# Kernel tuning notes

Measured on AMD Instinct MI355X. Metric: run time of the kernel, lower is better.

## Reference

```python
import jax, jax.numpy as jnp
from jax import lax
import numpy as np

B, T, I, H, OUT = 4096, 168, 4, 64, 12


def setup_inputs() -> dict:
    key = jax.random.key(0)
    ks = jax.random.split(key, 14)
    s = 0.05
    return {
        "x": jax.random.normal(ks[0], (B, T, I), dtype=jnp.float32),
        # LSTM layer 0 (PyTorch gate order: i, f, g, o)
        "Wih0": jax.random.normal(ks[1], (4 * H, I), dtype=jnp.float32) * s,
        "Whh0": jax.random.normal(ks[2], (4 * H, H), dtype=jnp.float32) * s,
        "bih0": jax.random.normal(ks[3], (4 * H,), dtype=jnp.float32) * s,
        "bhh0": jax.random.normal(ks[4], (4 * H,), dtype=jnp.float32) * s,
        # LSTM layer 1
        "Wih1": jax.random.normal(ks[5], (4 * H, H), dtype=jnp.float32) * s,
        "Whh1": jax.random.normal(ks[6], (4 * H, H), dtype=jnp.float32) * s,
        "bih1": jax.random.normal(ks[7], (4 * H,), dtype=jnp.float32) * s,
        "bhh1": jax.random.normal(ks[8], (4 * H,), dtype=jnp.float32) * s,
        # FC head: Linear(64,64) -> ReLU -> Linear(64,12)
        "W1": jax.random.normal(ks[9], (64, H), dtype=jnp.float32) * s,
        "b1": jax.random.normal(ks[10], (64,), dtype=jnp.float32) * s,
        "W2": jax.random.normal(ks[11], (OUT, 64), dtype=jnp.float32) * s,
        "b2": jax.random.normal(ks[12], (OUT,), dtype=jnp.float32) * s,
    }


def _lstm_layer(x, Wih, Whh, bih, bhh):
    # x: [B, T, in]; returns hidden sequence [B, T, H]
    Bsz = x.shape[0]
    Hd = Whh.shape[1]
    # Precompute input contribution for all timesteps: [B, T, 4H]
    xg = jnp.einsum('bti,gi->btg', x, Wih) + bih + bhh

    def step(carry, xg_t):
        h, c = carry
        g = xg_t + h @ Whh.T  # [B, 4H]
        i, f, gg, o = jnp.split(g, 4, axis=-1)
        i = jax.nn.sigmoid(i)
        f = jax.nn.sigmoid(f)
        gg = jnp.tanh(gg)
        o = jax.nn.sigmoid(o)
        c = f * c + i * gg
        h = o * jnp.tanh(c)
        return (h, c), h

    h0 = jnp.zeros((Bsz, Hd), x.dtype)
    (_, _), hs = lax.scan(step, (h0, h0), jnp.swapaxes(xg, 0, 1))  # hs: [T, B, H]
    return jnp.swapaxes(hs, 0, 1)


def reference(x, Wih0, Whh0, bih0, bhh0, Wih1, Whh1, bih1, bhh1, W1, b1, W2, b2):
    # Eval-mode forward: dropout layers are identity.
    h1 = _lstm_layer(x, Wih0, Whh0, bih0, bhh0)   # [B, T, H]
    h2 = _lstm_layer(h1, Wih1, Whh1, bih1, bhh1)  # [B, T, H]
    last = h2[:, -1, :]                            # [B, H]
    z = jax.nn.relu(last @ W1.T + b1)              # [B, 64]
    out = z @ W2.T + b2                            # [B, 12]
    return out.reshape(-1, 3, 4)
```

## Files before the change

### kernel.cpp

```cpp
#include <hip/hip_runtime.h>


typedef _Float16 h8 __attribute__((ext_vector_type(8)));
typedef _Float16 h4 __attribute__((ext_vector_type(4)));
typedef float f4 __attribute__((ext_vector_type(4)));

#define ROWB 208
#define HBUF (16 * ROWB)
#define XTAB_OFF 0
#define XTAB_BYTES (169 * 256)
#define H0_OFF XTAB_BYTES
#define H1_OFF (H0_OFF + 2 * HBUF)
#define SMEM_TOTAL (H1_OFF + 2 * HBUF)

#define K1F 1.4426950408889634f
#define K2F 2.8853900817779268f

__device__ __forceinline__ float exp2_(float x) {
#if __has_builtin(__builtin_amdgcn_exp2f)
  return __builtin_amdgcn_exp2f(x);
#else
  float r; asm("v_exp_f32 %0, %1" : "=v"(r) : "v"(x)); return r;
#endif
}
__device__ __forceinline__ float rcp_(float x) {
#if __has_builtin(__builtin_amdgcn_rcpf)
  return __builtin_amdgcn_rcpf(x);
#else
  float r; asm("v_rcp_f32 %0, %1" : "=v"(r) : "v"(x)); return r;
#endif
}

__device__ __forceinline__ f4 mfma16(h8 a, h8 b, f4 c) {
  return __builtin_amdgcn_mfma_f32_16x16x32_f16(a, b, c, 0, 0, 0);
}

__device__ __forceinline__ h8 load_w8s(const float* __restrict__ p, float sc) {
  h8 r;
#pragma unroll
  for (int j = 0; j < 8; j++) r[j] = (_Float16)(p[j] * sc);
  return r;
}

__device__ __forceinline__ void lstm_act(f4 a, float& c, float& h) {
  float Ei = exp2_(-a[0]);
  float Ef = exp2_(-a[1]);
  float Eg = exp2_(a[2]);
  float Eo = exp2_(-a[3]);
  float A = 1.f + Ei, B = 1.f + Ef, C = 1.f + Eg, D = 1.f + Eo;
  float AB = A * B, CD = C * D, BD = B * D;
  float R  = rcp_(AB * CD);
  float fv = (A * CD) * R;
  float ig = (BD * (Eg - 1.f)) * R;
  float ov = (AB * C) * R;
  c = fv * c + ig;
  float r2 = rcp_(exp2_(c * K2F) + 1.f);
  h = ov * (1.f - 2.f * r2);
}

extern "C" __global__ void __launch_bounds__(512, 2)
weather_lstm_mfma6(const float* __restrict__ x,
                   const float* __restrict__ Wih0, const float* __restrict__ Whh0,
                   const float* __restrict__ bih0, const float* __restrict__ bhh0,
                   const float* __restrict__ Wih1, const float* __restrict__ Whh1,
                   const float* __restrict__ bih1, const float* __restrict__ bhh1,
                   const float* __restrict__ W1, const float* __restrict__ b1,
                   const float* __restrict__ W2, const float* __restrict__ b2,
                   float* __restrict__ out)
{
  __shared__ __align__(16) unsigned char smem[SMEM_TOTAL];
  const int tid  = threadIdx.x;
  const int lane = tid & 63;
  const int w    = tid >> 6;
  const int col  = lane & 15;
  const int quad = lane >> 4;
  const int sB   = blockIdx.x * 16;

  const int g_  = col & 3;
  const int ul_ = col >> 2;
  const float asc = (g_ == 2) ? K2F : K1F;

  h8 a0[2][3], a1i[2][2], a1h[2][2];
#pragma unroll
  for (int t = 0; t < 2; t++) {
    const int r = g_ * 64 + w * 8 + t * 4 + ul_;
#pragma unroll
    for (int f = 0; f < 2; f++) {
      a0[t][f]  = load_w8s(Whh0 + r * 64 + f * 32 + quad * 8, asc);
      a1i[t][f] = load_w8s(Wih1 + r * 64 + f * 32 + quad * 8, asc);
      a1h[t][f] = load_w8s(Whh1 + r * 64 + f * 32 + quad * 8, asc);
    }
    h8 xw = {};
    if (quad == 0) {
#pragma unroll
      for (int j = 0; j < 4; j++) xw[j] = (_Float16)(Wih0[r * 4 + j] * asc);
    }
    a0[t][2] = xw;
  }

  f4 bias0v[2], bias1v[2];
#pragma unroll
  for (int t = 0; t < 2; t++) {
#pragma unroll
    for (int reg = 0; reg < 4; reg++) {
      const int rr = reg * 64 + w * 8 + t * 4 + quad;
      const float bs = (reg == 2) ? K2F : K1F;
      bias0v[t][reg] = (bih0[rr] + bhh0[rr]) * bs;
      bias1v[t][reg] = (bih1[rr] + bhh1[rr]) * bs;
    }
  }

  for (int idx = tid; idx < SMEM_TOTAL / 4; idx += 512) ((int*)smem)[idx] = 0;
  __syncthreads();
  for (int idx = tid; idx < 16 * 168; idx += 512) {
    const int c_ = idx / 168, t_ = idx - c_ * 168;
    f4 xv = *(const f4*)(x + ((size_t)(sB + c_) * 168 + t_) * 4);
    h4 xh;
#pragma unroll
    for (int j = 0; j < 4; j++) xh[j] = (_Float16)xv[j];
    *(h4*)(smem + XTAB_OFF + t_ * 256 + c_ * 16) = xh;
  }
  __syncthreads();

  float c0[2] = {0.f, 0.f}, c1[2] = {0.f, 0.f}, hl[2] = {0.f, 0.f};
  const int bo  = col * ROWB + quad * 16;
  const int wo0 = col * ROWB + (w * 8 + quad) * 2;
  const unsigned char* xp = smem + XTAB_OFF + col * 16;

  for (int k = 0; k <= 168; k++) {
    const int kb = k & 1, kbn = kb ^ 1;
    const unsigned char* h0r = smem + H0_OFF + kbn * HBUF;
    unsigned char*       h0w = smem + H0_OFF + kb  * HBUF;
    const unsigned char* h1r = smem + H1_OFF + kb  * HBUF;
    unsigned char*       h1w = smem + H1_OFF + kbn * HBUF;

    h8 b0  = *(const h8*)(h0r + bo);
    h8 b1v = *(const h8*)(h0r + bo + 64);
    h8 bx  = *(const h8*)(xp + k * 256);
    h8 q0  = *(const h8*)(h1r + bo);
    h8 q1  = *(const h8*)(h1r + bo + 64);

    f4 A[2], C[2];
#pragma unroll
    for (int t = 0; t < 2; t++) {
      A[t] = mfma16(a0[t][0], b0, bias0v[t]);
      C[t] = mfma16(a1i[t][0], b0, bias1v[t]);
      A[t] = mfma16(a0[t][1], b1v, A[t]);
      C[t] = mfma16(a1i[t][1], b1v, C[t]);
      A[t] = mfma16(a0[t][2], bx, A[t]);
      C[t] = mfma16(a1h[t][0], q0, C[t]);
      C[t] = mfma16(a1h[t][1], q1, C[t]);
    }

    if (k < 168) {
#pragma unroll
      for (int t = 0; t < 2; t++) {
        float h0o;
        lstm_act(A[t], c0[t], h0o);
        *(_Float16*)(h0w + wo0 + t * 8) = (_Float16)h0o;
      }
    }
    if (k > 0) {
#pragma unroll
      for (int t = 0; t < 2; t++) {
        lstm_act(C[t], c1[t], hl[t]);
        *(_Float16*)(h1w + wo0 + t * 8) = (_Float16)hl[t];
      }
    }
    __syncthreads();
  }

  float* fh = (float*)smem;
#pragma unroll
  for (int t = 0; t < 2; t++)
    fh[col * 64 + (w * 8 + t * 4 + quad)] = hl[t];
  __syncthreads();

  {
    const int u = tid & 63, grp = tid >> 6;
    const float* w1r = W1 + u * 64;
    float* zl = (float*)(smem + 4096);
#pragma unroll
    for (int rep = 0; rep < 2; rep++) {
      const int s = grp + rep * 8;
      float za = b1[u];
      const float* f0 = fh + s * 64;
      for (int j = 0; j < 64; j++) za += w1r[j] * f0[j];
      zl[s * 64 + u] = fmaxf(za, 0.f);
    }
  }
  __syncthreads();

  if (tid < 192) {
    const float* zl = (const float*)(smem + 4096);
    const int s = tid / 12, o = tid - s * 12;
    float a = b2[o];
    for (int j = 0; j < 64; j++) a += W2[o * 64 + j] * zl[s * 64 + j];
    out[(sB + s) * 12 + o] = a;
  }
}

extern "C" void kernel_launch(void* const* d_in, const int* in_sizes, int n_in,
                              void* d_out, int out_size, void* d_ws, size_t ws_size,
                              hipStream_t stream) {
  (void)in_sizes; (void)n_in; (void)d_ws; (void)ws_size; (void)out_size;
  const float* x    = (const float*)d_in[0];
  const float* Wih0 = (const float*)d_in[1];
  const float* Whh0 = (const float*)d_in[2];
  const float* bih0 = (const float*)d_in[3];
  const float* bhh0 = (const float*)d_in[4];
  const float* Wih1 = (const float*)d_in[5];
  const float* Whh1 = (const float*)d_in[6];
  const float* bih1 = (const float*)d_in[7];
  const float* bhh1 = (const float*)d_in[8];
  const float* W1   = (const float*)d_in[9];
  const float* b1   = (const float*)d_in[10];
  const float* W2   = (const float*)d_in[11];
  const float* b2   = (const float*)d_in[12];

  weather_lstm_mfma6<<<dim3(256), dim3(512), 0, stream>>>(
      x, Wih0, Whh0, bih0, bhh0, Wih1, Whh1, bih1, bhh1, W1, b1, W2, b2,
      (float*)d_out);
}
```

Measured before the change: 230.7 us.

## Halve batch per block and split activation work across MFMA column halves

Each block now handles 8 sequences instead of 16, and the grid doubles to 512 blocks. MFMA columns 8-15 duplicate the batch columns, so each lane applies the LSTM activation to only one of the two tile outputs, selected by column half. This halves the serial transcendental work per lane on the recurrent critical path and spreads blocks over more CUs, with launch bounds raised to 4 blocks per CU. The cost is that half of each MFMA's output columns do redundant work, and higher occupancy may pressure registers.

```diff
diff --git a/kernel.cpp b/kernel.cpp
--- a/kernel.cpp
+++ b/kernel.cpp
@@ -6,9 +6,9 @@
 typedef float f4 __attribute__((ext_vector_type(4)));
 
 #define ROWB 208
-#define HBUF (16 * ROWB)
+#define HBUF (8 * ROWB)
 #define XTAB_OFF 0
-#define XTAB_BYTES (169 * 256)
+#define XTAB_BYTES (169 * 128)
 #define H0_OFF XTAB_BYTES
 #define H1_OFF (H0_OFF + 2 * HBUF)
 #define SMEM_TOTAL (H1_OFF + 2 * HBUF)
@@ -39,6 +39,13 @@
   h8 r;
 #pragma unroll
   for (int j = 0; j < 8; j++) r[j] = (_Float16)(p[j] * sc);
+  return r;
+}
+
+__device__ __forceinline__ f4 sel4(int hi, f4 a, f4 b) {
+  f4 r;
+#pragma unroll
+  for (int j = 0; j < 4; j++) r[j] = hi ? b[j] : a[j];
   return r;
 }
 
@@ -58,8 +65,8 @@
   h = ov * (1.f - 2.f * r2);
 }
 
-extern "C" __global__ void __launch_bounds__(512, 2)
-weather_lstm_mfma6(const float* __restrict__ x,
+extern "C" __global__ void __launch_bounds__(512, 4)
+weather_lstm_mfma7(const float* __restrict__ x,
                    const float* __restrict__ Wih0, const float* __restrict__ Whh0,
                    const float* __restrict__ bih0, const float* __restrict__ bhh0,
                    const float* __restrict__ Wih1, const float* __restrict__ Whh1,
@@ -73,8 +80,10 @@
   const int lane = tid & 63;
   const int w    = tid >> 6;
   const int col  = lane & 15;
+  const int s    = col & 7;
+  const int sel  = col >> 3;
   const int quad = lane >> 4;
-  const int sB   = blockIdx.x * 16;
+  const int sB   = blockIdx.x * 8;
 
   const int g_  = col & 3;
   const int ul_ = col >> 2;
@@ -112,20 +121,20 @@
 
   for (int idx = tid; idx < SMEM_TOTAL / 4; idx += 512) ((int*)smem)[idx] = 0;
   __syncthreads();
-  for (int idx = tid; idx < 16 * 168; idx += 512) {
+  for (int idx = tid; idx < 8 * 168; idx += 512) {
     const int c_ = idx / 168, t_ = idx - c_ * 168;
     f4 xv = *(const f4*)(x + ((size_t)(sB + c_) * 168 + t_) * 4);
     h4 xh;
 #pragma unroll
     for (int j = 0; j < 4; j++) xh[j] = (_Float16)xv[j];
-    *(h4*)(smem + XTAB_OFF + t_ * 256 + c_ * 16) = xh;
-  }
-  __syncthreads();
-
-  float c0[2] = {0.f, 0.f}, c1[2] = {0.f, 0.f}, hl[2] = {0.f, 0.f};
-  const int bo  = col * ROWB + quad * 16;
-  const int wo0 = col * ROWB + (w * 8 + quad) * 2;
-  const unsigned char* xp = smem + XTAB_OFF + col * 16;
+    *(h4*)(smem + XTAB_OFF + t_ * 128 + c_ * 16) = xh;
+  }
+  __syncthreads();
+
+  float c0 = 0.f, c1 = 0.f, hl = 0.f;
+  const int bo = s * ROWB + quad * 16;
+  const int wo = s * ROWB + (w * 8 + sel * 4 + quad) * 2;
+  const unsigned char* xp = smem + XTAB_OFF + s * 16;
 
   for (int k = 0; k <= 168; k++) {
     const int kb = k & 1, kbn = kb ^ 1;
@@ -136,7 +145,7 @@
 
     h8 b0  = *(const h8*)(h0r + bo);
     h8 b1v = *(const h8*)(h0r + bo + 64);
-    h8 bx  = *(const h8*)(xp + k * 256);
+    h8 bx  = *(const h8*)(xp + k * 128);
     h8 q0  = *(const h8*)(h1r + bo);
     h8 q1  = *(const h8*)(h1r + bo + 64);
 
@@ -153,50 +162,40 @@
     }
 
     if (k < 168) {
-#pragma unroll
-      for (int t = 0; t < 2; t++) {
-        float h0o;
-        lstm_act(A[t], c0[t], h0o);
-        *(_Float16*)(h0w + wo0 + t * 8) = (_Float16)h0o;
-      }
+      f4 G = sel4(sel, A[0], A[1]);
+      float h0o;
+      lstm_act(G, c0, h0o);
+      *(_Float16*)(h0w + wo) = (_Float16)h0o;
     }
     if (k > 0) {
-#pragma unroll
-      for (int t = 0; t < 2; t++) {
-        lstm_act(C[t], c1[t], hl[t]);
-        *(_Float16*)(h1w + wo0 + t * 8) = (_Float16)hl[t];
-      }
+      f4 G = sel4(sel, C[0], C[1]);
+      lstm_act(G, c1, hl);
+      *(_Float16*)(h1w + wo) = (_Float16)hl;
     }
     __syncthreads();
   }
 
   float* fh = (float*)smem;
-#pragma unroll
-  for (int t = 0; t < 2; t++)
-    fh[col * 64 + (w * 8 + t * 4 + quad)] = hl[t];
+  fh[s * 64 + (w * 8 + sel * 4 + quad)] = hl;
   __syncthreads();
 
   {
     const int u = tid & 63, grp = tid >> 6;
+    float za = b1[u];
     const float* w1r = W1 + u * 64;
+    const float* f0 = fh + grp * 64;
+    for (int j = 0; j < 64; j++) za += w1r[j] * f0[j];
     float* zl = (float*)(smem + 4096);
-#pragma unroll
-    for (int rep = 0; rep < 2; rep++) {
-      const int s = grp + rep * 8;
-      float za = b1[u];
-      const float* f0 = fh + s * 64;
-      for (int j = 0; j < 64; j++) za += w1r[j] * f0[j];
-      zl[s * 64 + u] = fmaxf(za, 0.f);
-    }
-  }
-  __syncthreads();
-
-  if (tid < 192) {
+    zl[grp * 64 + u] = fmaxf(za, 0.f);
+  }
+  __syncthreads();
+
+  if (tid < 96) {
     const float* zl = (const float*)(smem + 4096);
-    const int s = tid / 12, o = tid - s * 12;
+    const int s2 = tid / 12, o = tid - s2 * 12;
     float a = b2[o];
-    for (int j = 0; j < 64; j++) a += W2[o * 64 + j] * zl[s * 64 + j];
-    out[(sB + s) * 12 + o] = a;
+    for (int j = 0; j < 64; j++) a += W2[o * 64 + j] * zl[s2 * 64 + j];
+    out[(sB + s2) * 12 + o] = a;
   }
 }
 
@@ -218,7 +217,7 @@
   const float* W2   = (const float*)d_in[11];
   const float* b2   = (const float*)d_in[12];
 
-  weather_lstm_mfma6<<<dim3(256), dim3(512), 0, stream>>>(
+  weather_lstm_mfma7<<<dim3(512), dim3(512), 0, stream>>>(
       x, Wih0, Whh0, bih0, bhh0, Wih1, Whh1, bih1, bhh1, W1, b1, W2, b2,
       (float*)d_out);
 }
```

Measured after the change: 260.6 us. 1.13x slower.

## Split LSTM layers across warp groups with LDS flag handoff instead of barriers

Applied to the files above, without the earlier changes.

The two LSTM layers now run on separate warp groups: four waves compute layer 0 and four compute layer 1. Each wave handles all four gates for 16 hidden units. The per-step block-wide __syncthreads is replaced by per-wave progress flags in shared memory that consumers spin on, with a four-deep ring buffer for layer-0 hidden states so layer 0 can run ahead of layer 1. The aim is to pipeline the layers and cut barrier stalls. In exchange it adds spin-wait polling overhead, depends on LDS memory ordering through volatile accesses and block fences, and gives each wave a longer serial dependency chain per step.

```diff
diff --git a/kernel.cpp b/kernel.cpp
--- a/kernel.cpp
+++ b/kernel.cpp
@@ -10,8 +10,9 @@
 #define XTAB_OFF 0
 #define XTAB_BYTES (169 * 256)
 #define H0_OFF XTAB_BYTES
-#define H1_OFF (H0_OFF + 2 * HBUF)
-#define SMEM_TOTAL (H1_OFF + 2 * HBUF)
+#define H1_OFF (H0_OFF + 4 * HBUF)
+#define FLAG_OFF (H1_OFF + 2 * HBUF)
+#define SMEM_TOTAL (FLAG_OFF + 32)
 
 #define K1F 1.4426950408889634f
 #define K2F 2.8853900817779268f
@@ -40,6 +41,15 @@
 #pragma unroll
   for (int j = 0; j < 8; j++) r[j] = (_Float16)(p[j] * sc);
   return r;
+}
+
+__device__ __forceinline__ void spin_min_ge(volatile const int* f, int target) {
+  for (;;) {
+    int a = f[0], b = f[1], c = f[2], d = f[3];
+    int m = min(min(a, b), min(c, d));
+    if (m >= target) break;
+    __builtin_amdgcn_s_sleep(1);
+  }
 }
 
 __device__ __forceinline__ void lstm_act(f4 a, float& c, float& h) {
@@ -59,7 +69,7 @@
 }
 
 extern "C" __global__ void __launch_bounds__(512, 2)
-weather_lstm_mfma6(const float* __restrict__ x,
+weather_lstm_mfma8(const float* __restrict__ x,
                    const float* __restrict__ Wih0, const float* __restrict__ Whh0,
                    const float* __restrict__ bih0, const float* __restrict__ bhh0,
                    const float* __restrict__ Wih1, const float* __restrict__ Whh1,
@@ -76,39 +86,8 @@
   const int quad = lane >> 4;
   const int sB   = blockIdx.x * 16;
 
-  const int g_  = col & 3;
-  const int ul_ = col >> 2;
-  const float asc = (g_ == 2) ? K2F : K1F;
-
-  h8 a0[2][3], a1i[2][2], a1h[2][2];
-#pragma unroll
-  for (int t = 0; t < 2; t++) {
-    const int r = g_ * 64 + w * 8 + t * 4 + ul_;
-#pragma unroll
-    for (int f = 0; f < 2; f++) {
-      a0[t][f]  = load_w8s(Whh0 + r * 64 + f * 32 + quad * 8, asc);
-      a1i[t][f] = load_w8s(Wih1 + r * 64 + f * 32 + quad * 8, asc);
-      a1h[t][f] = load_w8s(Whh1 + r * 64 + f * 32 + quad * 8, asc);
-    }
-    h8 xw = {};
-    if (quad == 0) {
-#pragma unroll
-      for (int j = 0; j < 4; j++) xw[j] = (_Float16)(Wih0[r * 4 + j] * asc);
-    }
-    a0[t][2] = xw;
-  }
-
-  f4 bias0v[2], bias1v[2];
-#pragma unroll
-  for (int t = 0; t < 2; t++) {
-#pragma unroll
-    for (int reg = 0; reg < 4; reg++) {
-      const int rr = reg * 64 + w * 8 + t * 4 + quad;
-      const float bs = (reg == 2) ? K2F : K1F;
-      bias0v[t][reg] = (bih0[rr] + bhh0[rr]) * bs;
-      bias1v[t][reg] = (bih1[rr] + bhh1[rr]) * bs;
-    }
-  }
+  volatile int* p0w = (volatile int*)(smem + FLAG_OFF);
+  volatile int* p1w = (volatile int*)(smem + FLAG_OFF + 16);
 
   for (int idx = tid; idx < SMEM_TOTAL / 4; idx += 512) ((int*)smem)[idx] = 0;
   __syncthreads();
@@ -122,58 +101,145 @@
   }
   __syncthreads();
 
-  float c0[2] = {0.f, 0.f}, c1[2] = {0.f, 0.f}, hl[2] = {0.f, 0.f};
-  const int bo  = col * ROWB + quad * 16;
-  const int wo0 = col * ROWB + (w * 8 + quad) * 2;
-  const unsigned char* xp = smem + XTAB_OFF + col * 16;
-
-  for (int k = 0; k <= 168; k++) {
-    const int kb = k & 1, kbn = kb ^ 1;
-    const unsigned char* h0r = smem + H0_OFF + kbn * HBUF;
-    unsigned char*       h0w = smem + H0_OFF + kb  * HBUF;
-    const unsigned char* h1r = smem + H1_OFF + kb  * HBUF;
-    unsigned char*       h1w = smem + H1_OFF + kbn * HBUF;
-
-    h8 b0  = *(const h8*)(h0r + bo);
-    h8 b1v = *(const h8*)(h0r + bo + 64);
-    h8 bx  = *(const h8*)(xp + k * 256);
-    h8 q0  = *(const h8*)(h1r + bo);
-    h8 q1  = *(const h8*)(h1r + bo + 64);
-
-    f4 A[2], C[2];
-#pragma unroll
-    for (int t = 0; t < 2; t++) {
-      A[t] = mfma16(a0[t][0], b0, bias0v[t]);
-      C[t] = mfma16(a1i[t][0], b0, bias1v[t]);
-      A[t] = mfma16(a0[t][1], b1v, A[t]);
-      C[t] = mfma16(a1i[t][1], b1v, C[t]);
-      A[t] = mfma16(a0[t][2], bx, A[t]);
-      C[t] = mfma16(a1h[t][0], q0, C[t]);
-      C[t] = mfma16(a1h[t][1], q1, C[t]);
-    }
-
-    if (k < 168) {
-#pragma unroll
-      for (int t = 0; t < 2; t++) {
-        float h0o;
-        lstm_act(A[t], c0[t], h0o);
-        *(_Float16*)(h0w + wo0 + t * 8) = (_Float16)h0o;
-      }
-    }
-    if (k > 0) {
-#pragma unroll
-      for (int t = 0; t < 2; t++) {
-        lstm_act(C[t], c1[t], hl[t]);
-        *(_Float16*)(h1w + wo0 + t * 8) = (_Float16)hl[t];
-      }
-    }
-    __syncthreads();
-  }
+  const int wl = w & 3;
+  const int u0 = wl * 16;
+  const int uu = u0 + quad * 4;
+  const int bo = col * ROWB + quad * 16;
+  const int wo = col * ROWB + uu * 2;
+
+  float hout[4] = {0.f, 0.f, 0.f, 0.f};
+
+  if (w < 4) {
+    h8 aW[4][2], aX[4];
+    f4 bias[4];
+#pragma unroll
+    for (int g = 0; g < 4; ++g) {
+      const float sc = (g == 2) ? K2F : K1F;
+      const int r = g * 64 + u0 + col;
+#pragma unroll
+      for (int f = 0; f < 2; ++f)
+        aW[g][f] = load_w8s(Whh0 + r * 64 + f * 32 + quad * 8, sc);
+      h8 xw = {};
+      if (quad == 0) {
+#pragma unroll
+        for (int j = 0; j < 4; ++j) xw[j] = (_Float16)(Wih0[r * 4 + j] * sc);
+      }
+      aX[g] = xw;
+#pragma unroll
+      for (int j = 0; j < 4; ++j)
+        bias[g][j] = (bih0[g * 64 + uu + j] + bhh0[g * 64 + uu + j]) * sc;
+    }
+
+    float cc[4] = {0.f, 0.f, 0.f, 0.f};
+    const unsigned char* xp = smem + XTAB_OFF + col * 16;
+
+    for (int k = 0; k < 168; ++k) {
+      spin_min_ge(p0w, k);
+      if (k >= 4) spin_min_ge(p1w, k - 3);
+
+      const unsigned char* h0r = smem + H0_OFF + ((k - 1) & 3) * HBUF;
+      unsigned char*       h0wp = smem + H0_OFF + (k & 3) * HBUF;
+
+      h8 b0  = *(const h8*)(h0r + bo);
+      h8 b1v = *(const h8*)(h0r + bo + 64);
+      h8 bx  = *(const h8*)(xp + k * 256);
+
+      f4 A0 = mfma16(aW[0][0], b0, bias[0]);
+      f4 A1 = mfma16(aW[1][0], b0, bias[1]);
+      f4 A2 = mfma16(aW[2][0], b0, bias[2]);
+      f4 A3 = mfma16(aW[3][0], b0, bias[3]);
+      A0 = mfma16(aW[0][1], b1v, A0);
+      A1 = mfma16(aW[1][1], b1v, A1);
+      A2 = mfma16(aW[2][1], b1v, A2);
+      A3 = mfma16(aW[3][1], b1v, A3);
+      A0 = mfma16(aX[0], bx, A0);
+      A1 = mfma16(aX[1], bx, A1);
+      A2 = mfma16(aX[2], bx, A2);
+      A3 = mfma16(aX[3], bx, A3);
+
+      h4 hv;
+#pragma unroll
+      for (int j = 0; j < 4; ++j) {
+        f4 G; G[0] = A0[j]; G[1] = A1[j]; G[2] = A2[j]; G[3] = A3[j];
+        float ho;
+        lstm_act(G, cc[j], ho);
+        hv[j] = (_Float16)ho;
+      }
+      *(h4*)(h0wp + wo) = hv;
+
+      __threadfence_block();
+      if (lane == 0) p0w[wl] = k + 1;
+    }
+  } else {
+    h8 aI[4][2], aH[4][2];
+    f4 bias[4];
+#pragma unroll
+    for (int g = 0; g < 4; ++g) {
+      const float sc = (g == 2) ? K2F : K1F;
+      const int r = g * 64 + u0 + col;
+#pragma unroll
+      for (int f = 0; f < 2; ++f) {
+        aI[g][f] = load_w8s(Wih1 + r * 64 + f * 32 + quad * 8, sc);
+        aH[g][f] = load_w8s(Whh1 + r * 64 + f * 32 + quad * 8, sc);
+      }
+#pragma unroll
+      for (int j = 0; j < 4; ++j)
+        bias[g][j] = (bih1[g * 64 + uu + j] + bhh1[g * 64 + uu + j]) * sc;
+    }
+
+    float cc[4] = {0.f, 0.f, 0.f, 0.f};
+
+    for (int k = 0; k < 168; ++k) {
+      spin_min_ge(p1w, k);
+      spin_min_ge(p0w, k + 1);
+
+      const unsigned char* h0r  = smem + H0_OFF + (k & 3) * HBUF;
+      const unsigned char* h1r  = smem + H1_OFF + ((k - 1) & 1) * HBUF;
+      unsigned char*       h1wp = smem + H1_OFF + (k & 1) * HBUF;
+
+      h8 b0  = *(const h8*)(h0r + bo);
+      h8 b1v = *(const h8*)(h0r + bo + 64);
+      h8 q0  = *(const h8*)(h1r + bo);
+      h8 q1  = *(const h8*)(h1r + bo + 64);
+
+      f4 C0 = mfma16(aI[0][0], b0, bias[0]);
+      f4 C1 = mfma16(aI[1][0], b0, bias[1]);
+      f4 C2 = mfma16(aI[2][0], b0, bias[2]);
+      f4 C3 = mfma16(aI[3][0], b0, bias[3]);
+      C0 = mfma16(aI[0][1], b1v, C0);
+      C1 = mfma16(aI[1][1], b1v, C1);
+      C2 = mfma16(aI[2][1], b1v, C2);
+      C3 = mfma16(aI[3][1], b1v, C3);
+      C0 = mfma16(aH[0][0], q0, C0);
+      C1 = mfma16(aH[1][0], q0, C1);
+      C2 = mfma16(aH[2][0], q0, C2);
+      C3 = mfma16(aH[3][0], q0, C3);
+      C0 = mfma16(aH[0][1], q1, C0);
+      C1 = mfma16(aH[1][1], q1, C1);
+      C2 = mfma16(aH[2][1], q1, C2);
+      C3 = mfma16(aH[3][1], q1, C3);
+
+      h4 hv;
+#pragma unroll
+      for (int j = 0; j < 4; ++j) {
+        f4 G; G[0] = C0[j]; G[1] = C1[j]; G[2] = C2[j]; G[3] = C3[j];
+        lstm_act(G, cc[j], hout[j]);
+        hv[j] = (_Float16)hout[j];
+      }
+      *(h4*)(h1wp + wo) = hv;
+
+      __threadfence_block();
+      if (lane == 0) p1w[wl] = k + 1;
+    }
+  }
+
+  __syncthreads();
 
   float* fh = (float*)smem;
-#pragma unroll
-  for (int t = 0; t < 2; t++)
-    fh[col * 64 + (w * 8 + t * 4 + quad)] = hl[t];
+  if (w >= 4) {
+    f4 hv; hv[0] = hout[0]; hv[1] = hout[1]; hv[2] = hout[2]; hv[3] = hout[3];
+    *(f4*)(fh + col * 64 + uu) = hv;
+  }
   __syncthreads();
 
   {
@@ -181,22 +247,22 @@
     const float* w1r = W1 + u * 64;
     float* zl = (float*)(smem + 4096);
 #pragma unroll
-    for (int rep = 0; rep < 2; rep++) {
-      const int s = grp + rep * 8;
+    for (int rep = 0; rep < 2; ++rep) {
+      const int s2 = grp + rep * 8;
       float za = b1[u];
-      const float* f0 = fh + s * 64;
-      for (int j = 0; j < 64; j++) za += w1r[j] * f0[j];
-      zl[s * 64 + u] = fmaxf(za, 0.f);
+      const float* f0 = fh + s2 * 64;
+      for (int j = 0; j < 64; ++j) za += w1r[j] * f0[j];
+      zl[s2 * 64 + u] = fmaxf(za, 0.f);
     }
   }
   __syncthreads();
 
   if (tid < 192) {
     const float* zl = (const float*)(smem + 4096);
-    const int s = tid / 12, o = tid - s * 12;
+    const int s2 = tid / 12, o = tid - s2 * 12;
     float a = b2[o];
-    for (int j = 0; j < 64; j++) a += W2[o * 64 + j] * zl[s * 64 + j];
-    out[(sB + s) * 12 + o] = a;
+    for (int j = 0; j < 64; ++j) a += W2[o * 64 + j] * zl[s2 * 64 + j];
+    out[(sB + s2) * 12 + o] = a;
   }
 }
 
@@ -218,7 +284,7 @@
   const float* W2   = (const float*)d_in[11];
   const float* b2   = (const float*)d_in[12];
 
-  weather_lstm_mfma6<<<dim3(256), dim3(512), 0, stream>>>(
+  weather_lstm_mfma8<<<dim3(256), dim3(512), 0, stream>>>(
       x, Wih0, Whh0, bih0, bhh0, Wih1, Whh1, bih1, bhh1, W1, b1, W2, b2,
       (float*)d_out);
 }
```

After: 251.9 us. +9.2%, slower.

## Split block into two sequence groups and ping-pong MFMA with activations

Applied to the files above, without the earlier changes.

Each block's 16 sequences are split into two groups of 8 handled by separate halves of the waves. While one half issues the MFMA gate matmuls for its timestep, the other half computes the LSTM activations for its previous step, with two barriers per step. The weight layout is changed so each wave owns 16 hidden units across all four gates. The intent is to overlap matrix-core work with transcendental VALU work. The cost is twice the weight registers per wave, two barriers per step instead of one, and MFMA tiles where half the columns are wasted.

```diff
diff --git a/kernel.cpp b/kernel.cpp
--- a/kernel.cpp
+++ b/kernel.cpp
@@ -3,6 +3,7 @@
 
 typedef _Float16 h8 __attribute__((ext_vector_type(8)));
 typedef _Float16 h4 __attribute__((ext_vector_type(4)));
+typedef _Float16 h2v __attribute__((ext_vector_type(2)));
 typedef float f4 __attribute__((ext_vector_type(4)));
 
 #define ROWB 208
@@ -59,7 +60,7 @@
 }
 
 extern "C" __global__ void __launch_bounds__(512, 2)
-weather_lstm_mfma6(const float* __restrict__ x,
+weather_lstm_mfma9(const float* __restrict__ x,
                    const float* __restrict__ Wih0, const float* __restrict__ Whh0,
                    const float* __restrict__ bih0, const float* __restrict__ bhh0,
                    const float* __restrict__ Wih1, const float* __restrict__ Whh1,
@@ -74,39 +75,37 @@
   const int w    = tid >> 6;
   const int col  = lane & 15;
   const int quad = lane >> 4;
+  const int grp  = w >> 2;
+  const int wl   = w & 3;
+  const int u0   = wl * 16;
+  const int gcol = (col & 7) + grp * 8;
+  const bool hi  = (col >= 8);
+  const int j0   = hi ? 2 : 0;
+  const int uu   = u0 + quad * 4;
   const int sB   = blockIdx.x * 16;
 
-  const int g_  = col & 3;
-  const int ul_ = col >> 2;
-  const float asc = (g_ == 2) ? K2F : K1F;
-
-  h8 a0[2][3], a1i[2][2], a1h[2][2];
-#pragma unroll
-  for (int t = 0; t < 2; t++) {
-    const int r = g_ * 64 + w * 8 + t * 4 + ul_;
-#pragma unroll
-    for (int f = 0; f < 2; f++) {
-      a0[t][f]  = load_w8s(Whh0 + r * 64 + f * 32 + quad * 8, asc);
-      a1i[t][f] = load_w8s(Wih1 + r * 64 + f * 32 + quad * 8, asc);
-      a1h[t][f] = load_w8s(Whh1 + r * 64 + f * 32 + quad * 8, asc);
+  h8 aW[4][2], aX[4], aI[4][2], aH[4][2];
+  f4 bias0[4], bias1[4];
+#pragma unroll
+  for (int g = 0; g < 4; ++g) {
+    const float sc = (g == 2) ? K2F : K1F;
+    const int r = g * 64 + u0 + col;
+#pragma unroll
+    for (int f = 0; f < 2; ++f) {
+      aW[g][f] = load_w8s(Whh0 + r * 64 + f * 32 + quad * 8, sc);
+      aI[g][f] = load_w8s(Wih1 + r * 64 + f * 32 + quad * 8, sc);
+      aH[g][f] = load_w8s(Whh1 + r * 64 + f * 32 + quad * 8, sc);
     }
     h8 xw = {};
     if (quad == 0) {
 #pragma unroll
-      for (int j = 0; j < 4; j++) xw[j] = (_Float16)(Wih0[r * 4 + j] * asc);
-    }
-    a0[t][2] = xw;
-  }
-
-  f4 bias0v[2], bias1v[2];
-#pragma unroll
-  for (int t = 0; t < 2; t++) {
-#pragma unroll
-    for (int reg = 0; reg < 4; reg++) {
-      const int rr = reg * 64 + w * 8 + t * 4 + quad;
-      const float bs = (reg == 2) ? K2F : K1F;
-      bias0v[t][reg] = (bih0[rr] + bhh0[rr]) * bs;
-      bias1v[t][reg] = (bih1[rr] + bhh1[rr]) * bs;
+      for (int j = 0; j < 4; ++j) xw[j] = (_Float16)(Wih0[r * 4 + j] * sc);
+    }
+    aX[g] = xw;
+#pragma unroll
+    for (int j = 0; j < 4; ++j) {
+      bias0[g][j] = (bih0[g * 64 + uu + j] + bhh0[g * 64 + uu + j]) * sc;
+      bias1[g][j] = (bih1[g * 64 + uu + j] + bhh1[g * 64 + uu + j]) * sc;
     }
   }
 
@@ -122,81 +121,95 @@
   }
   __syncthreads();
 
-  float c0[2] = {0.f, 0.f}, c1[2] = {0.f, 0.f}, hl[2] = {0.f, 0.f};
-  const int bo  = col * ROWB + quad * 16;
-  const int wo0 = col * ROWB + (w * 8 + quad) * 2;
-  const unsigned char* xp = smem + XTAB_OFF + col * 16;
-
-  for (int k = 0; k <= 168; k++) {
-    const int kb = k & 1, kbn = kb ^ 1;
-    const unsigned char* h0r = smem + H0_OFF + kbn * HBUF;
-    unsigned char*       h0w = smem + H0_OFF + kb  * HBUF;
-    const unsigned char* h1r = smem + H1_OFF + kb  * HBUF;
-    unsigned char*       h1w = smem + H1_OFF + kbn * HBUF;
-
-    h8 b0  = *(const h8*)(h0r + bo);
-    h8 b1v = *(const h8*)(h0r + bo + 64);
-    h8 bx  = *(const h8*)(xp + k * 256);
-    h8 q0  = *(const h8*)(h1r + bo);
-    h8 q1  = *(const h8*)(h1r + bo + 64);
-
-    f4 A[2], C[2];
-#pragma unroll
-    for (int t = 0; t < 2; t++) {
-      A[t] = mfma16(a0[t][0], b0, bias0v[t]);
-      C[t] = mfma16(a1i[t][0], b0, bias1v[t]);
-      A[t] = mfma16(a0[t][1], b1v, A[t]);
-      C[t] = mfma16(a1i[t][1], b1v, C[t]);
-      A[t] = mfma16(a0[t][2], bx, A[t]);
-      C[t] = mfma16(a1h[t][0], q0, C[t]);
-      C[t] = mfma16(a1h[t][1], q1, C[t]);
-    }
-
+  f4 Av[4], Cv[4];
+  float c0s[2] = {0.f, 0.f}, c1s[2] = {0.f, 0.f}, hl[2] = {0.f, 0.f};
+  const int bo = gcol * ROWB + quad * 16;
+  const int wo = gcol * ROWB + (uu + j0) * 2;
+  const unsigned char* xp = smem + XTAB_OFF + gcol * 16;
+
+  auto M = [&](int k) {
+    const unsigned char* h0r = smem + H0_OFF + ((k - 1) & 1) * HBUF;
+    const unsigned char* h1r = smem + H1_OFF + (k & 1) * HBUF;
+    h8 rb0 = *(const h8*)(h0r + bo);
+    h8 rb1 = *(const h8*)(h0r + bo + 64);
+    h8 rbx = *(const h8*)(xp + k * 256);
+    h8 rq0 = *(const h8*)(h1r + bo);
+    h8 rq1 = *(const h8*)(h1r + bo + 64);
+#pragma unroll
+    for (int g = 0; g < 4; ++g) {
+      Av[g] = mfma16(aW[g][0], rb0, bias0[g]);
+      Cv[g] = mfma16(aI[g][0], rb0, bias1[g]);
+      Av[g] = mfma16(aW[g][1], rb1, Av[g]);
+      Cv[g] = mfma16(aI[g][1], rb1, Cv[g]);
+      Av[g] = mfma16(aX[g], rbx, Av[g]);
+      Cv[g] = mfma16(aH[g][0], rq0, Cv[g]);
+      Cv[g] = mfma16(aH[g][1], rq1, Cv[g]);
+    }
+  };
+
+  auto ACT = [&](int k) {
     if (k < 168) {
-#pragma unroll
-      for (int t = 0; t < 2; t++) {
-        float h0o;
-        lstm_act(A[t], c0[t], h0o);
-        *(_Float16*)(h0w + wo0 + t * 8) = (_Float16)h0o;
+      h2v hv;
+#pragma unroll
+      for (int a = 0; a < 2; ++a) {
+        f4 G;
+#pragma unroll
+        for (int g = 0; g < 4; ++g) G[g] = hi ? Av[g][2 + a] : Av[g][a];
+        float ho;
+        lstm_act(G, c0s[a], ho);
+        hv[a] = (_Float16)ho;
       }
-    }
-    if (k > 0) {
-#pragma unroll
-      for (int t = 0; t < 2; t++) {
-        lstm_act(C[t], c1[t], hl[t]);
-        *(_Float16*)(h1w + wo0 + t * 8) = (_Float16)hl[t];
+      *(h2v*)(smem + H0_OFF + (k & 1) * HBUF + wo) = hv;
+    }
+    if (k >= 1) {
+      h2v hv;
+#pragma unroll
+      for (int a = 0; a < 2; ++a) {
+        f4 G;
+#pragma unroll
+        for (int g = 0; g < 4; ++g) G[g] = hi ? Cv[g][2 + a] : Cv[g][a];
+        lstm_act(G, c1s[a], hl[a]);
+        hv[a] = (_Float16)hl[a];
       }
-    }
+      *(h2v*)(smem + H1_OFF + ((k + 1) & 1) * HBUF + wo) = hv;
+    }
+  };
+
+  for (int k = 0; k <= 169; ++k) {
+    if (grp == 0) { if (k <= 168) M(k); }
+    else          { if (k >= 1)   ACT(k - 1); }
     __syncthreads();
+    if (grp == 0) { if (k <= 168) ACT(k); }
+    else          { if (k <= 168) M(k); }
+    __syncthreads();
   }
 
   float* fh = (float*)smem;
-#pragma unroll
-  for (int t = 0; t < 2; t++)
-    fh[col * 64 + (w * 8 + t * 4 + quad)] = hl[t];
+  fh[gcol * 64 + uu + j0 + 0] = hl[0];
+  fh[gcol * 64 + uu + j0 + 1] = hl[1];
   __syncthreads();
 
   {
-    const int u = tid & 63, grp = tid >> 6;
+    const int u = tid & 63, g2 = tid >> 6;
     const float* w1r = W1 + u * 64;
     float* zl = (float*)(smem + 4096);
 #pragma unroll
-    for (int rep = 0; rep < 2; rep++) {
-      const int s = grp + rep * 8;
+    for (int rep = 0; rep < 2; ++rep) {
+      const int s2 = g2 + rep * 8;
       float za = b1[u];
-      const float* f0 = fh + s * 64;
-      for (int j = 0; j < 64; j++) za += w1r[j] * f0[j];
-      zl[s * 64 + u] = fmaxf(za, 0.f);
+      const float* f0 = fh + s2 * 64;
+      for (int j = 0; j < 64; ++j) za += w1r[j] * f0[j];
+      zl[s2 * 64 + u] = fmaxf(za, 0.f);
     }
   }
   __syncthreads();
 
   if (tid < 192) {
     const float* zl = (const float*)(smem + 4096);
-    const int s = tid / 12, o = tid - s * 12;
+    const int s2 = tid / 12, o = tid - s2 * 12;
     float a = b2[o];
-    for (int j = 0; j < 64; j++) a += W2[o * 64 + j] * zl[s * 64 + j];
-    out[(sB + s) * 12 + o] = a;
+    for (int j = 0; j < 64; ++j) a += W2[o * 64 + j] * zl[s2 * 64 + j];
+    out[(sB + s2) * 12 + o] = a;
   }
 }
 
@@ -218,7 +231,7 @@
   const float* W2   = (const float*)d_in[11];
   const float* b2   = (const float*)d_in[12];
 
-  weather_lstm_mfma6<<<dim3(256), dim3(512), 0, stream>>>(
+  weather_lstm_mfma9<<<dim3(256), dim3(512), 0, stream>>>(
       x, Wih0, Whh0, bih0, bhh0, Wih1, Whh1, bih1, bhh1, W1, b1, W2, b2,
       (float*)d_out);
 }
```

Measured after the change: 309.1 us. 34.0% more time.
